# Optimization experiments

Hardware: AMD Instinct MI355X
Metric: run time of the kernel (lower is better)

## Reference

```python
import jax, jax.numpy as jnp
import numpy as np

ROUTINGS = 3

def _squash_size1(s):
    # Faithful to squash(tensor, dim=-1) applied on a size-1 last dim:
    # squared_norm degenerates to elementwise s**2.
    sq = s * s
    return (sq / (1.0 + sq)) * s / jnp.sqrt(sq + 1e-9)

def setup_inputs() -> dict:
    key = jax.random.key(0)
    k1, k2 = jax.random.split(key)
    B, I, Din = 16, 1152, 16
    N, D = 32, 64
    inputs = jax.random.normal(k1, (B, I, Din), dtype=jnp.float32)
    W = jax.random.normal(k2, (1, N, I, D, Din), dtype=jnp.float32)
    return {"inputs": inputs, "W": W}

def reference(inputs, W):
    # inputs: [B, I, Din]; W: [1, N, I, D, Din]
    # torch: matmul(W, inputs.unsqueeze(1).unsqueeze(4)) -> [B,N,I,D,1]; drop trailing 1.
    x_hat = jnp.einsum('nidk,bik->bnid', W[0], inputs)  # [B, N, I, D]
    b = jnp.zeros_like(x_hat)                            # [B, N, I, D] (quirk: carries D axis)
    outputs = None
    for i in range(ROUTINGS):
        c = jax.nn.softmax(b, axis=2)                    # softmax over input capsules
        s = jnp.sum(c * x_hat, axis=2)                   # [B, N, D]
        outputs = _squash_size1(s)                       # elementwise squash (size-1 dim quirk)
        if i < ROUTINGS - 1:
            # (inputs_hat * outputs).sum(dim=-1) over size-1 dim == elementwise product
            b = b + x_hat * outputs[:, :, None, :]
    return outputs[..., None]                            # [B, N, D, 1] (after squeeze(2))
```

## Files before the change

### kernel.cpp

```cpp
#include <hip/hip_runtime.h>
#include <hip/hip_bf16.h>
#include <math.h>

#define B_   16
#define N_   32
#define I_   1152
#define DIN  16
#define D_   64
#define TI   16
#define IB   (I_/TI)
#define IC   16
#define BND  (B_*N_*D_)

#if __has_builtin(__builtin_amdgcn_exp2f)
#define EXP2(x) __builtin_amdgcn_exp2f(x)
#else
#define EXP2(x) exp2f(x)
#endif

#define LOG2E 1.4426950408889634f

typedef __attribute__((ext_vector_type(8))) short short8v;
typedef __attribute__((ext_vector_type(4))) float f32x4;
typedef __attribute__((ext_vector_type(4))) unsigned int u32x4;
typedef __attribute__((ext_vector_type(2))) unsigned int u32x2;

__device__ __forceinline__ float squash1(float s) {
    float sq = s * s;
    return (sq / (1.0f + sq)) * s * rsqrtf(sq + 1e-9f);
}
__device__ __forceinline__ unsigned int bfh(float v) {
    return (unsigned int)__builtin_bit_cast(unsigned short, __float2bfloat16(v));
}
__device__ __forceinline__ float bff(unsigned int hi16) {
    return __builtin_bit_cast(float, hi16 << 16);
}

__global__ __launch_bounds__(256, 3) void k_xhat(const float* __restrict__ inp,
                                                 const float* __restrict__ W,
                                                 unsigned short* __restrict__ xh2,
                                                 float* __restrict__ part) {
    __shared__ __align__(16) unsigned short xs[4096];
    const int bx = blockIdx.x;
    const int n  = bx / IB;
    const int ib = bx % IB;
    const int i0 = ib * TI;
    const int t  = threadIdx.x;
    const int l  = t & 63;
    const int mt = t >> 6;
    const int row = l & 15;
    const int ko  = (l >> 4) & 1;
    const bool loHalf = (l >= 32);

    #pragma unroll
    for (int rep = 0; rep < 2; ++rep) {
        int s   = rep * 256 + t;
        int bb  = s >> 5;
        int il  = (s >> 1) & 15;
        int sko = s & 1;
        const float* src = inp + (size_t)bb * (I_ * DIN) + (size_t)(i0 + il) * DIN + sko * 8;
        f32x4 a0 = *(const f32x4*)src;
        f32x4 a1 = *(const f32x4*)(src + 4);
        u32x4 p;
        p.x = (bfh(a0.y) << 16) | bfh(a0.x);
        p.y = (bfh(a0.w) << 16) | bfh(a0.z);
        p.z = (bfh(a1.y) << 16) | bfh(a1.x);
        p.w = (bfh(a1.w) << 16) | bfh(a1.z);
        int base = (bb * 512 + il * 32 + sko * 16) ^ ((bb & 7) << 4);
        *(u32x4*)((char*)xs + base) = p;
    }
    __syncthreads();

    const float* wb = W + ((size_t)(n * I_ + i0) * 64 + mt * 16 + row) * 16 + ko * 8;

    unsigned int pk[TI * 2];
    f32x4 s0v = {0.f, 0.f, 0.f, 0.f};

#define LOADG(DST, C) {                                                        \
        _Pragma("unroll")                                                      \
        for (int j = 0; j < 4; ++j) {                                          \
            const f32x4* p = (const f32x4*)(wb + (size_t)((C) * 4 + j) * 1024);\
            DST[2 * j] = p[0]; DST[2 * j + 1] = p[1];                          \
        } }

#define COMPG(SRC, C) {                                                        \
        _Pragma("unroll")                                                      \
        for (int j = 0; j < 4; ++j) {                                          \
            const int i = (C) * 4 + j;                                         \
            int xaddr = ((l & 15) * 512 + i * 32 + ko * 16) ^ (((l & 15) & 7) << 4); \
            short8v bfrag = *(const short8v*)((const char*)xs + xaddr);        \
            short8v afrag;                                                     \
            _Pragma("unroll")                                                  \
            for (int q = 0; q < 8; ++q) {                                      \
                float wq = SRC[2 * j + (q >> 2)][q & 3];                       \
                unsigned int hi = bfh(wq);                                     \
                unsigned int lo = bfh(wq - bff(hi));                           \
                afrag[q] = (short)(loHalf ? lo : hi);                          \
            }                                                                  \
            f32x4 acc = __builtin_amdgcn_mfma_f32_16x16x32_bf16(               \
                afrag, bfrag, (f32x4){0.f, 0.f, 0.f, 0.f}, 0, 0, 0);           \
            s0v += acc;                                                        \
            pk[i * 2]     = (bfh(acc[1]) << 16) | bfh(acc[0]);                 \
            pk[i * 2 + 1] = (bfh(acc[3]) << 16) | bfh(acc[2]);                 \
        } }

    f32x4 wA[8], wB[8];
    LOADG(wA, 0)
    LOADG(wB, 1)
    COMPG(wA, 0)
    LOADG(wA, 2)
    COMPG(wB, 1)
    LOADG(wB, 3)
    COMPG(wA, 2)
    COMPG(wB, 3)
#undef LOADG
#undef COMPG

    size_t pidx = (((size_t)ib * B_ + (l & 15)) * N_ + n) * 64 + mt * 16 + (l >> 4) * 4;
    *(f32x4*)(part + pidx) = s0v;

    #pragma unroll
    for (int i = 0; i < TI; ++i) {
        u32x2 v;
        v.x = pk[i * 2];
        v.y = pk[i * 2 + 1];
        size_t off = (size_t)(n * I_ + i0 + i) * 1024 + (size_t)t * 4;
        *reinterpret_cast<u32x2*>(xh2 + off) = v;
    }
}

__global__ __launch_bounds__(256) void k_out0(const float* __restrict__ part,
                                              float* __restrict__ coef) {
    const int t = blockIdx.x * 256 + threadIdx.x;
    float s = 0.0f;
    for (int j = 0; j < IB; ++j) s += part[(size_t)j * BND + t];
    s *= (1.0f / (float)I_);
    coef[t] = squash1(s);
}

__global__ __launch_bounds__(256) void k_rpart(const unsigned short* __restrict__ xh2,
                                               const float* __restrict__ coef,
                                               float* __restrict__ part2) {
    const int bx = blockIdx.x;
    const int n  = bx >> 4;
    const int ic = bx & 15;
    const int t  = threadIdx.x;
    const int b  = t & 15;
    const int d0 = (t >> 4) * 4;

    const unsigned short* base = xh2 + ((size_t)n * I_ + (size_t)ic * (I_ / IC)) * 1024
                               + (size_t)t * 4;
    f32x4 c4 = *(const f32x4*)(coef + ((size_t)b * N_ + n) * 64 + d0);
    float c2[4] = {c4.x * LOG2E, c4.y * LOG2E, c4.z * LOG2E, c4.w * LOG2E};
    float z[4] = {0, 0, 0, 0}, a[4] = {0, 0, 0, 0};

    #pragma unroll 8
    for (int i = 0; i < I_ / IC; ++i) {
        u32x2 u = *(const u32x2*)(base + (size_t)i * 1024);
        unsigned short s4[4] = {(unsigned short)(u.x & 0xffffu), (unsigned short)(u.x >> 16),
                                (unsigned short)(u.y & 0xffffu), (unsigned short)(u.y >> 16)};
        #pragma unroll
        for (int j = 0; j < 4; ++j) {
            float x = bff(s4[j]);
            float e = EXP2(x * c2[j]);
            z[j] += e;
            a[j] = fmaf(e, x, a[j]);
        }
    }

    size_t pidx = ((((size_t)ic * N_ + n) * 16 + b) * 64 + d0) * 2;
    f32x4 v0 = {z[0], a[0], z[1], a[1]};
    f32x4 v1 = {z[2], a[2], z[3], a[3]};
    *(f32x4*)(part2 + pidx)     = v0;
    *(f32x4*)(part2 + pidx + 4) = v1;
}

__global__ __launch_bounds__(256) void k_rfin(const float* __restrict__ part2,
                                              const float* __restrict__ coefIn,
                                              float* __restrict__ outp,
                                              int final_) {
    const int gid = blockIdx.x * 256 + threadIdx.x;
    float Z = 0.0f, A = 0.0f;
    #pragma unroll
    for (int ic = 0; ic < IC; ++ic) {
        const float* p = part2 + ((size_t)ic * BND + gid) * 2;
        Z += p[0];
        A += p[1];
    }
    const int d = gid & 63, b = (gid >> 6) & 15, n = gid >> 10;
    const int ci = (b * N_ + n) * D_ + d;
    float o = squash1(A / Z);
    outp[ci] = final_ ? o : (coefIn[ci] + o);
}

extern "C" void kernel_launch(void* const* d_in, const int* in_sizes, int n_in,
                              void* d_out, int out_size, void* d_ws, size_t ws_size,
                              hipStream_t stream) {
    const float* inp = (const float*)d_in[0];
    const float* W   = (const float*)d_in[1];
    float* out = (float*)d_out;

    unsigned short* xh2 = (unsigned short*)d_ws;
    float* part  = (float*)((char*)d_ws + 75497472);
    float* part2 = (float*)((char*)d_ws + 84934656);
    float* coef  = (float*)((char*)d_ws + 89128960);

    k_xhat<<<dim3(N_ * IB), dim3(256), 0, stream>>>(inp, W, xh2, part);
    k_out0<<<dim3(BND / 256), dim3(256), 0, stream>>>(part, coef);
    k_rpart<<<dim3(N_ * IC), dim3(256), 0, stream>>>(xh2, coef, part2);
    k_rfin <<<dim3(BND / 256), dim3(256), 0, stream>>>(part2, coef, coef, 0);
    k_rpart<<<dim3(N_ * IC), dim3(256), 0, stream>>>(xh2, coef, part2);
    k_rfin <<<dim3(BND / 256), dim3(256), 0, stream>>>(part2, coef, out, 1);
}
```

Measured before the change: 76.63 us.

## Stream W through double-buffered LDS with async global_load_lds in xhat kernel

The x_hat kernel stops loading W tiles straight into registers. It now issues direct global-to-LDS 16-byte async loads into a two-stage LDS buffer with an XOR swizzle, then reads the A fragments back from LDS. Barriers separate the stages so the next chunk loads while the current one is computed. The occupancy hint rises from 3 to 4 blocks per CU, which the larger LDS footprint must still allow. The goal is to cut register pressure and raise bandwidth on the large W stream, at the cost of extra LDS traffic, barriers and reliance on correct wait counts for the async loads.

Measured after the change: 77.62 us. No clear change (+1.3%).

```diff
diff --git a/kernel.cpp b/kernel.cpp
--- a/kernel.cpp
+++ b/kernel.cpp
@@ -36,11 +36,17 @@
     return __builtin_bit_cast(float, hi16 << 16);
 }
 
-__global__ __launch_bounds__(256, 3) void k_xhat(const float* __restrict__ inp,
+#define GL16(g, l) __builtin_amdgcn_global_load_lds(                          \
+    (const __attribute__((address_space(1))) void*)(g),                       \
+    (__attribute__((address_space(3))) void*)(l), 16, 0, 0)
+
+__global__ __launch_bounds__(256, 4) void k_xhat(const float* __restrict__ inp,
                                                  const float* __restrict__ W,
                                                  unsigned short* __restrict__ xh2,
                                                  float* __restrict__ part) {
     __shared__ __align__(16) unsigned short xs[4096];
+    __shared__ __align__(16) float wls[2][4096];
+
     const int bx = blockIdx.x;
     const int n  = bx / IB;
     const int ib = bx % IB;
@@ -48,9 +54,47 @@
     const int t  = threadIdx.x;
     const int l  = t & 63;
     const int mt = t >> 6;
-    const int row = l & 15;
-    const int ko  = (l >> 4) & 1;
+    const int ko = (l >> 4) & 1;
     const bool loHalf = (l >= 32);
+    const int dd = mt * 16 + (l & 15);
+    const int A_OFF   = (dd * 64 + ko * 32) ^ (((dd >> 1) & 3) << 4);
+    const int lane_sw = (l * 16) ^ (((l >> 3) & 3) << 4);
+
+    const char* Wn = (const char*)(W + (size_t)(n * I_ + i0) * 1024);
+
+#define STAGE(c) {                                                             \
+        _Pragma("unroll")                                                      \
+        for (int r = 0; r < 4; ++r) {                                          \
+            const char* g = Wn + (size_t)((c) * 4 + r) * 4096 + mt * 1024 + lane_sw; \
+            char* ld = (char*)wls[(c) & 1] + r * 4096 + mt * 1024;             \
+            GL16(g, ld);                                                       \
+        } }
+
+#define COMPQ(c) {                                                             \
+        const char* wq = (const char*)wls[(c) & 1];                            \
+        _Pragma("unroll")                                                      \
+        for (int j = 0; j < 4; ++j) {                                          \
+            const int i = (c) * 4 + j;                                         \
+            f32x4 wk0 = *(const f32x4*)(wq + j * 4096 + A_OFF);                \
+            f32x4 wk1 = *(const f32x4*)(wq + j * 4096 + (A_OFF ^ 16));         \
+            int xaddr = ((l & 15) * 512 + i * 32 + ko * 16) ^ (((l & 15) & 7) << 4); \
+            short8v bfrag = *(const short8v*)((const char*)xs + xaddr);        \
+            short8v afrag;                                                     \
+            _Pragma("unroll")                                                  \
+            for (int q = 0; q < 8; ++q) {                                      \
+                float wv = (q < 4) ? wk0[q] : wk1[q - 4];                      \
+                unsigned int hi = bfh(wv);                                     \
+                unsigned int lo = bfh(wv - bff(hi));                           \
+                afrag[q] = (short)(loHalf ? lo : hi);                          \
+            }                                                                  \
+            f32x4 acc = __builtin_amdgcn_mfma_f32_16x16x32_bf16(               \
+                afrag, bfrag, (f32x4){0.f, 0.f, 0.f, 0.f}, 0, 0, 0);           \
+            s0v += acc;                                                        \
+            pk[i * 2]     = (bfh(acc[1]) << 16) | bfh(acc[0]);                 \
+            pk[i * 2 + 1] = (bfh(acc[3]) << 16) | bfh(acc[2]);                 \
+        } }
+
+    STAGE(0)
 
     #pragma unroll
     for (int rep = 0; rep < 2; ++rep) {
@@ -71,50 +115,15 @@
     }
     __syncthreads();
 
-    const float* wb = W + ((size_t)(n * I_ + i0) * 64 + mt * 16 + row) * 16 + ko * 8;
-
     unsigned int pk[TI * 2];
     f32x4 s0v = {0.f, 0.f, 0.f, 0.f};
 
-#define LOADG(DST, C) {                                                        \
-        _Pragma("unroll")                                                      \
-        for (int j = 0; j < 4; ++j) {                                          \
-            const f32x4* p = (const f32x4*)(wb + (size_t)((C) * 4 + j) * 1024);\
-            DST[2 * j] = p[0]; DST[2 * j + 1] = p[1];                          \
-        } }
-
-#define COMPG(SRC, C) {                                                        \
-        _Pragma("unroll")                                                      \
-        for (int j = 0; j < 4; ++j) {                                          \
-            const int i = (C) * 4 + j;                                         \
-            int xaddr = ((l & 15) * 512 + i * 32 + ko * 16) ^ (((l & 15) & 7) << 4); \
-            short8v bfrag = *(const short8v*)((const char*)xs + xaddr);        \
-            short8v afrag;                                                     \
-            _Pragma("unroll")                                                  \
-            for (int q = 0; q < 8; ++q) {                                      \
-                float wq = SRC[2 * j + (q >> 2)][q & 3];                       \
-                unsigned int hi = bfh(wq);                                     \
-                unsigned int lo = bfh(wq - bff(hi));                           \
-                afrag[q] = (short)(loHalf ? lo : hi);                          \
-            }                                                                  \
-            f32x4 acc = __builtin_amdgcn_mfma_f32_16x16x32_bf16(               \
-                afrag, bfrag, (f32x4){0.f, 0.f, 0.f, 0.f}, 0, 0, 0);           \
-            s0v += acc;                                                        \
-            pk[i * 2]     = (bfh(acc[1]) << 16) | bfh(acc[0]);                 \
-            pk[i * 2 + 1] = (bfh(acc[3]) << 16) | bfh(acc[2]);                 \
-        } }
-
-    f32x4 wA[8], wB[8];
-    LOADG(wA, 0)
-    LOADG(wB, 1)
-    COMPG(wA, 0)
-    LOADG(wA, 2)
-    COMPG(wB, 1)
-    LOADG(wB, 3)
-    COMPG(wA, 2)
-    COMPG(wB, 3)
-#undef LOADG
-#undef COMPG
+    STAGE(1) COMPQ(0) __syncthreads();
+    STAGE(2) COMPQ(1) __syncthreads();
+    STAGE(3) COMPQ(2) __syncthreads();
+    COMPQ(3)
+#undef STAGE
+#undef COMPQ
 
     size_t pidx = (((size_t)ib * B_ + (l & 15)) * N_ + n) * 64 + mt * 16 + (l >> 4) * 4;
     *(f32x4*)(part + pidx) = s0v;
```
